# Performance work log

Measured on AMD Instinct MI355X. Metric: run time of the kernel, lower is better.

## Reference

```python
import jax, jax.numpy as jnp
import numpy as np

N_SEQ, MAX_LEN, H_DIM, N_CHAR = 8, 4096, 1024, 256


def setup_inputs() -> dict:
    key = jax.random.key(0)
    ks = jax.random.split(key, 10)
    n_char_ev = 32768
    L, E = 12, 16384
    char_i_seq = jax.random.randint(ks[0], (n_char_ev,), 0, N_SEQ)
    char_i_pos = jax.random.randint(ks[1], (n_char_ev,), 0, MAX_LEN)
    char_ids = jax.random.randint(ks[2], (n_char_ev,), 0, N_CHAR)
    grp_i_seq = jax.random.randint(ks[3], (L, E), 0, N_SEQ)
    grp_i_first = jax.random.randint(ks[4], (L, E), 0, MAX_LEN)
    grp_i_second = jax.random.randint(ks[5], (L, E), 0, MAX_LEN)
    grp_i_pos = jax.random.randint(ks[6], (L, E), 0, MAX_LEN)
    # Learned params: embedding table (std = 1/sqrt(h_dim)) and composer Linear(2h -> h)
    emb_char = jax.random.normal(ks[7], (N_CHAR, H_DIM), dtype=jnp.float32) * (1.0 / H_DIM ** 0.5)
    W = jax.random.normal(ks[8], (2 * H_DIM, H_DIM), dtype=jnp.float32) * (1.0 / (2 * H_DIM) ** 0.5)
    b = jnp.zeros((H_DIM,), dtype=jnp.float32)
    return {"char_i_seq": char_i_seq, "char_i_pos": char_i_pos, "char_ids": char_ids,
            "grp_i_seq": grp_i_seq, "grp_i_first": grp_i_first, "grp_i_second": grp_i_second,
            "grp_i_pos": grp_i_pos, "emb_char": emb_char, "W": W, "b": b}


def reference(char_i_seq, char_i_pos, char_ids, grp_i_seq, grp_i_first,
              grp_i_second, grp_i_pos, emb_char, W, b):
    # h_frag: [n_seq, max_len, h_dim]
    h = jnp.zeros((N_SEQ, MAX_LEN, H_DIM), dtype=emb_char.dtype)
    # Leaf characters: embedding lookup + scatter-add
    h = h.at[char_i_seq, char_i_pos].add(emb_char[char_ids])

    def composer(left, right):
        # tanh(Linear(concat(left, right))) : [E, 2h] @ [2h, h] -> [E, h]
        return jnp.tanh(jnp.concatenate([left, right], axis=-1) @ W + b)

    def level_step(h, idx):
        i_seq, i_first, i_second, i_pos = idx
        out = composer(h[i_seq, i_first], h[i_seq, i_second])  # gather -> compose
        return h.at[i_seq, i_pos].add(out), None                # scatter-add

    h, _ = jax.lax.scan(level_step, h, (grp_i_seq, grp_i_first, grp_i_second, grp_i_pos))
    h = h.at[:, 0].set(0.0)  # h_frag[:, 0].fill_(0)
    return h
```

## Files before the change

### kernel.cpp

```cpp
#include <hip/hip_runtime.h>

#define NS 8
#define ML 4096
#define HD 1024
#define K2 2048
#define NEV 32768
#define NLEV 12
#define NE 16384
#define NSLOT (NS * ML)
#define CAP 8
#define BK 64
#define NT (K2 / BK)
#define LDS_BYTES 131072

typedef __attribute__((ext_vector_type(8))) short bf16x8;
typedef __attribute__((ext_vector_type(4))) float f32x4;

typedef __attribute__((address_space(1))) const void cvoid_g;
typedef __attribute__((address_space(3))) void void_l;

static __device__ __forceinline__ void load_lds_16(const void* g, void* l) {
    __builtin_amdgcn_global_load_lds((cvoid_g*)g, (void_l*)l, 16, 0, 0);
}

static __device__ __forceinline__ unsigned short f2bf(float f) {
    unsigned u = __float_as_uint(f);
    unsigned r = (u + 0x7fffu + ((u >> 16) & 1u)) >> 16;
    return (unsigned short)r;
}

static __device__ __forceinline__ float fast_tanh(float x) {
    return 1.0f - 2.0f / (__expf(2.0f * x) + 1.0f);
}

__global__ void wt_kernel(const float* __restrict__ W, unsigned short* __restrict__ WbT) {
    __shared__ unsigned short tile[64][65];
    const int t = threadIdx.x;
    const int k0 = blockIdx.x * 64;
    const int n0 = blockIdx.y * 64;
#pragma unroll
    for (int i = 0; i < 16; i++) {
        int idx = i * 256 + t;
        int r = idx >> 6, c = idx & 63;
        tile[r][c] = f2bf(W[(size_t)(k0 + r) * HD + n0 + c]);
    }
    __syncthreads();
#pragma unroll
    for (int i = 0; i < 16; i++) {
        int idx = i * 256 + t;
        int r = idx >> 6, c = idx & 63;
        WbT[(size_t)(n0 + r) * K2 + k0 + c] = tile[c][r];
    }
}

__global__ void char_ticket(const int* __restrict__ cseq, const int* __restrict__ cpos,
                            int* __restrict__ counts, int* __restrict__ ticket,
                            int* __restrict__ evlist) {
    const int e = blockIdx.x * 256 + threadIdx.x;
    if (e >= NEV) return;
    const int slot = cseq[e] * ML + cpos[e];
    const int t = atomicAdd(&counts[slot], 1);
    ticket[e] = t;
    if (t < CAP) evlist[slot * CAP + t] = e;
}

__global__ void char_slot_sum(const int* __restrict__ counts, const int* __restrict__ evlist,
                              const int* __restrict__ cid, const float* __restrict__ emb,
                              float* __restrict__ h) {
    const int slot = blockIdx.x;
    const int t = threadIdx.x;
    int n = counts[slot];
    if (n > CAP) n = CAP;
    float4 acc = {0.f, 0.f, 0.f, 0.f};
    for (int i = 0; i < n; i++) {
        const int e = evlist[slot * CAP + i];
        const int id = cid[e];
        const float4 v = ((const float4*)(emb + (size_t)id * HD))[t];
        acc.x += v.x; acc.y += v.y; acc.z += v.z; acc.w += v.w;
    }
    ((float4*)(h + (size_t)slot * HD))[t] = acc;
}

__global__ void char_overflow(const int* __restrict__ cseq, const int* __restrict__ cpos,
                              const int* __restrict__ cid, const int* __restrict__ ticket,
                              const float* __restrict__ emb, float* __restrict__ h) {
    const int e0 = blockIdx.x * 128;
    const int t = threadIdx.x;
    for (int i = 0; i < 128; i++) {
        const int e = e0 + i;
        if (ticket[e] < CAP) continue;
        const int slot = cseq[e] * ML + cpos[e];
        const int id = cid[e];
        const float4 v = ((const float4*)(emb + (size_t)id * HD))[t];
        float* dst = h + (size_t)slot * HD + t * 4;
        atomicAdd(dst + 0, v.x);
        atomicAdd(dst + 1, v.y);
        atomicAdd(dst + 2, v.z);
        atomicAdd(dst + 3, v.w);
    }
}

__global__ void grp_count(const int* __restrict__ iseq, const int* __restrict__ ipos,
                          int* __restrict__ gcounts) {
    const int idx = blockIdx.x * 256 + threadIdx.x;
    if (idx >= NLEV * NE) return;
    const int lev = idx >> 14;
    atomicAdd(&gcounts[lev * NSLOT + iseq[idx] * ML + ipos[idx]], 1);
}

__global__ void grp_dup(const int* __restrict__ iseq, const int* __restrict__ ipos,
                        const int* __restrict__ gcounts, unsigned char* __restrict__ dup) {
    const int idx = blockIdx.x * 256 + threadIdx.x;
    if (idx >= NLEV * NE) return;
    const int lev = idx >> 14;
    dup[idx] = (gcounts[lev * NSLOT + iseq[idx] * ML + ipos[idx]] > 1) ? 1 : 0;
}

__global__ void gather_x(const float* __restrict__ h, const int* __restrict__ iseq,
                         const int* __restrict__ ifirst, const int* __restrict__ isecond,
                         unsigned short* __restrict__ X) {
    const int e = blockIdx.x;
    const int t = threadIdx.x;
    const int seq = iseq[e], f = ifirst[e], s = isecond[e];
    const float4 a = ((const float4*)(h + ((size_t)seq * ML + f) * HD))[t];
    const float4 b = ((const float4*)(h + ((size_t)seq * ML + s) * HD))[t];
    ushort4 pa, pb;
    pa.x = f2bf(a.x); pa.y = f2bf(a.y); pa.z = f2bf(a.z); pa.w = f2bf(a.w);
    pb.x = f2bf(b.x); pb.y = f2bf(b.y); pb.z = f2bf(b.z); pb.w = f2bf(b.w);
    *(ushort4*)(X + (size_t)e * K2 + t * 4) = pa;
    *(ushort4*)(X + (size_t)e * K2 + HD + t * 4) = pb;
}

__global__ __launch_bounds__(512, 2) void gemm_scatter(
    const unsigned short* __restrict__ X,
    const unsigned short* __restrict__ WbT,
    const float* __restrict__ bias,
    const int* __restrict__ iseq, const int* __restrict__ ipos,
    const unsigned char* __restrict__ dup,
    float* __restrict__ h) {
    extern __shared__ unsigned short lds[];
    const int t = threadIdx.x;
    const int lane = t & 63;
    const int w = t >> 6;
    const int wm = w >> 2;
    const int wn = (w & 3) * 64;
    const int fr = lane & 15, fq = lane >> 4;

    const int bid = blockIdx.x;
    const int xcd = bid & 7, bix = bid >> 3;
    const int row0 = ((xcd & 1) * 32 + bix) * 256;
    const int col0 = (xcd >> 1) * 256;

    const int tr = t >> 3;
    const int sp = (t & 7) ^ (tr & 7);
    const unsigned short* Asrc = X + (size_t)(row0 + tr) * K2 + sp * 8;
    const unsigned short* Bsrc = WbT + (size_t)(col0 + tr) * K2 + sp * 8;

    f32x4 acc[8][4];
#pragma unroll
    for (int i = 0; i < 8; i++)
#pragma unroll
        for (int j = 0; j < 4; j++) acc[i][j] = (f32x4){0.f, 0.f, 0.f, 0.f};

    {
        unsigned short* dA = lds;
        unsigned short* dB = lds + 16384;
#pragma unroll
        for (int i = 0; i < 4; i++)
            load_lds_16(Asrc + (size_t)(i * 64) * K2, &dA[(i * 512 + t) * 8]);
#pragma unroll
        for (int i = 0; i < 4; i++)
            load_lds_16(Bsrc + (size_t)(i * 64) * K2, &dB[(i * 512 + t) * 8]);
    }

    for (int kt = 0; kt < NT; kt++) {
        const int d = kt & 1;
        if (kt + 1 < NT) {
            unsigned short* dA = lds + (d ^ 1) * 32768;
            unsigned short* dB = dA + 16384;
            const size_t ko = (size_t)(kt + 1) * BK;
#pragma unroll
            for (int i = 0; i < 4; i++)
                load_lds_16(Asrc + (size_t)(i * 64) * K2 + ko, &dA[(i * 512 + t) * 8]);
#pragma unroll
            for (int i = 0; i < 4; i++)
                load_lds_16(Bsrc + (size_t)(i * 64) * K2 + ko, &dB[(i * 512 + t) * 8]);
            asm volatile("s_waitcnt vmcnt(8)" ::: "memory");
        } else {
            asm volatile("s_waitcnt vmcnt(0)" ::: "memory");
        }
        __builtin_amdgcn_s_barrier();
        asm volatile("" ::: "memory");

        const unsigned short* sA = lds + d * 32768;
        const unsigned short* sB = sA + 16384;
#pragma unroll
        for (int ks = 0; ks < 2; ks++) {
            const int qs = ((ks * 4 + fq) ^ (fr & 7)) * 8;
            bf16x8 af[8], bfr[4];
#pragma unroll
            for (int mt = 0; mt < 8; mt++)
                af[mt] = *(const bf16x8*)&sA[(wm * 128 + mt * 16 + fr) * BK + qs];
#pragma unroll
            for (int nt = 0; nt < 4; nt++)
                bfr[nt] = *(const bf16x8*)&sB[(wn + nt * 16 + fr) * BK + qs];
            __builtin_amdgcn_s_setprio(1);
#pragma unroll
            for (int mt = 0; mt < 8; mt++)
#pragma unroll
                for (int nt = 0; nt < 4; nt++)
                    acc[mt][nt] = __builtin_amdgcn_mfma_f32_16x16x32_bf16(
                        af[mt], bfr[nt], acc[mt][nt], 0, 0, 0);
            __builtin_amdgcn_s_setprio(0);
        }
        asm volatile("" ::: "memory");
        __builtin_amdgcn_s_barrier();
    }

    float bv[4];
#pragma unroll
    for (int ni = 0; ni < 4; ni++) bv[ni] = bias[col0 + wn + ni * 16 + fr];
#pragma unroll
    for (int mi = 0; mi < 8; mi++) {
#pragma unroll
        for (int r = 0; r < 4; r++) {
            const int e = row0 + wm * 128 + mi * 16 + fq * 4 + r;
            const int seq = iseq[e], pos = ipos[e];
            float* hrow = h + ((size_t)seq * ML + pos) * HD + col0 + wn;
            if (dup[e]) {
#pragma unroll
                for (int ni = 0; ni < 4; ni++) {
                    float x = fast_tanh(acc[mi][ni][r] + bv[ni]);
                    atomicAdd(&hrow[ni * 16 + fr], x);
                }
            } else {
#pragma unroll
                for (int ni = 0; ni < 4; ni++) {
                    float x = fast_tanh(acc[mi][ni][r] + bv[ni]);
                    hrow[ni * 16 + fr] += x;
                }
            }
        }
    }
}

__global__ void zero_first(float* __restrict__ h) {
    const int t = blockIdx.x * 256 + threadIdx.x;
    const int seq = t >> 10, d = t & 1023;
    h[(size_t)seq * ML * HD + d] = 0.0f;
}

extern "C" void kernel_launch(void* const* d_in, const int* in_sizes, int n_in,
                              void* d_out, int out_size, void* d_ws, size_t ws_size,
                              hipStream_t stream) {
    const int* char_i_seq = (const int*)d_in[0];
    const int* char_i_pos = (const int*)d_in[1];
    const int* char_ids   = (const int*)d_in[2];
    const int* grp_i_seq    = (const int*)d_in[3];
    const int* grp_i_first  = (const int*)d_in[4];
    const int* grp_i_second = (const int*)d_in[5];
    const int* grp_i_pos    = (const int*)d_in[6];
    const float* emb = (const float*)d_in[7];
    const float* W   = (const float*)d_in[8];
    const float* b   = (const float*)d_in[9];
    float* h = (float*)d_out;

    unsigned short* WbT = (unsigned short*)d_ws;
    unsigned short* X   = (unsigned short*)((char*)d_ws + (8u << 20));
    int* counts = (int*)((char*)d_ws + (72u << 20));
    int* ticket = (int*)((char*)d_ws + (72u << 20) + (1u << 18));
    int* evlist = (int*)((char*)d_ws + (72u << 20) + (1u << 19));
    int* gcounts = (int*)((char*)d_ws + (74u << 20));
    unsigned char* gdup = (unsigned char*)((char*)d_ws + (76u << 20));

    static bool attr_done = false;
    if (!attr_done) {
        (void)hipFuncSetAttribute((const void*)gemm_scatter,
                                  hipFuncAttributeMaxDynamicSharedMemorySize, LDS_BYTES);
        attr_done = true;
    }

    hipMemsetAsync(counts, 0, NSLOT * sizeof(int), stream);
    hipMemsetAsync(gcounts, 0, (size_t)NLEV * NSLOT * sizeof(int), stream);
    wt_kernel<<<dim3(32, 16), 256, 0, stream>>>(W, WbT);
    char_ticket<<<NEV / 256, 256, 0, stream>>>(char_i_seq, char_i_pos, counts, ticket, evlist);
    char_slot_sum<<<NSLOT, 256, 0, stream>>>(counts, evlist, char_ids, emb, h);
    char_overflow<<<NEV / 128, 256, 0, stream>>>(char_i_seq, char_i_pos, char_ids, ticket, emb, h);
    grp_count<<<(NLEV * NE) / 256, 256, 0, stream>>>(grp_i_seq, grp_i_pos, gcounts);
    grp_dup<<<(NLEV * NE) / 256, 256, 0, stream>>>(grp_i_seq, grp_i_pos, gcounts, gdup);

    for (int lev = 0; lev < NLEV; lev++) {
        const int* iseq = grp_i_seq + lev * NE;
        const int* ifir = grp_i_first + lev * NE;
        const int* isec = grp_i_second + lev * NE;
        const int* ipos = grp_i_pos + lev * NE;
        gather_x<<<NE, 256, 0, stream>>>(h, iseq, ifir, isec, X);
        gemm_scatter<<<dim3(256), 512, LDS_BYTES, stream>>>(X, WbT, b, iseq, ipos,
                                                            gdup + lev * NE, h);
    }
    zero_first<<<32, 256, 0, stream>>>(h);
}
```

Measured before the change: 1.578 ms.

## Shrink GEMM tile to 256x128 with BK=32 triple-buffered LDS pipeline

Restructures the per-level GEMM from 256x256 tiles with BK=64 double buffering to 256x128 tiles with BK=32 and a three-stage LDS ring. The grid grows to 512 blocks and LDS drops to 72KB, so more blocks can be resident per CU. Prefetches are issued two k-steps ahead, after the fragment reads, which hides load latency and removes one barrier per iteration. The cost is more A-tile reloads, since each A tile is now fetched by twice as many column blocks, a lower MFMA-to-load ratio per k-step, and a changed block-to-XCD mapping that loses the old L2 locality swizzle.

```diff
diff --git a/kernel.cpp b/kernel.cpp
--- a/kernel.cpp
+++ b/kernel.cpp
@@ -9,9 +9,10 @@
 #define NE 16384
 #define NSLOT (NS * ML)
 #define CAP 8
-#define BK 64
+#define BK 32
 #define NT (K2 / BK)
-#define LDS_BYTES 131072
+#define TILE_ELEMS 12288
+#define LDS_BYTES 73728
 
 typedef __attribute__((ext_vector_type(8))) short bf16x8;
 typedef __attribute__((ext_vector_type(4))) float f32x4;
@@ -131,7 +132,7 @@
     *(ushort4*)(X + (size_t)e * K2 + HD + t * 4) = pb;
 }
 
-__global__ __launch_bounds__(512, 2) void gemm_scatter(
+__global__ __launch_bounds__(512, 4) void gemm_scatter(
     const unsigned short* __restrict__ X,
     const unsigned short* __restrict__ WbT,
     const float* __restrict__ bias,
@@ -143,83 +144,79 @@
     const int lane = t & 63;
     const int w = t >> 6;
     const int wm = w >> 2;
-    const int wn = (w & 3) * 64;
+    const int wn = (w & 3) * 32;
     const int fr = lane & 15, fq = lane >> 4;
 
     const int bid = blockIdx.x;
-    const int xcd = bid & 7, bix = bid >> 3;
-    const int row0 = ((xcd & 1) * 32 + bix) * 256;
-    const int col0 = (xcd >> 1) * 256;
-
-    const int tr = t >> 3;
-    const int sp = (t & 7) ^ (tr & 7);
-    const unsigned short* Asrc = X + (size_t)(row0 + tr) * K2 + sp * 8;
-    const unsigned short* Bsrc = WbT + (size_t)(col0 + tr) * K2 + sp * 8;
-
-    f32x4 acc[8][4];
+    const int col0 = (bid & 7) * 128;
+    const int row0 = (bid >> 3) * 256;
+
+    const int src_c = (t & 3) ^ ((t >> 3) & 3);
+    const unsigned short* Asrc = X + (size_t)(row0 + (t >> 2)) * K2 + src_c * 8;
+    const unsigned short* Bsrc = WbT + (size_t)(col0 + (t >> 2)) * K2 + src_c * 8;
+
+    f32x4 acc[8][2];
 #pragma unroll
     for (int i = 0; i < 8; i++)
 #pragma unroll
-        for (int j = 0; j < 4; j++) acc[i][j] = (f32x4){0.f, 0.f, 0.f, 0.f};
-
-    {
-        unsigned short* dA = lds;
-        unsigned short* dB = lds + 16384;
-#pragma unroll
-        for (int i = 0; i < 4; i++)
-            load_lds_16(Asrc + (size_t)(i * 64) * K2, &dA[(i * 512 + t) * 8]);
-#pragma unroll
-        for (int i = 0; i < 4; i++)
-            load_lds_16(Bsrc + (size_t)(i * 64) * K2, &dB[(i * 512 + t) * 8]);
-    }
+        for (int j = 0; j < 2; j++) acc[i][j] = (f32x4){0.f, 0.f, 0.f, 0.f};
+
+    unsigned short* b0 = lds;
+    unsigned short* b1 = lds + TILE_ELEMS;
+    unsigned short* b2 = lds + 2 * TILE_ELEMS;
+
+    load_lds_16(Asrc, &b0[t * 8]);
+    load_lds_16(Asrc + (size_t)128 * K2, &b0[(512 + t) * 8]);
+    load_lds_16(Bsrc, &b0[8192 + t * 8]);
+    load_lds_16(Asrc + BK, &b1[t * 8]);
+    load_lds_16(Asrc + (size_t)128 * K2 + BK, &b1[(512 + t) * 8]);
+    load_lds_16(Bsrc + BK, &b1[8192 + t * 8]);
+    asm volatile("s_waitcnt vmcnt(3)" ::: "memory");
+    __builtin_amdgcn_s_barrier();
+    asm volatile("" ::: "memory");
+
+    const int slot8 = (fq ^ ((fr >> 1) & 3)) * 8;
 
     for (int kt = 0; kt < NT; kt++) {
-        const int d = kt & 1;
-        if (kt + 1 < NT) {
-            unsigned short* dA = lds + (d ^ 1) * 32768;
-            unsigned short* dB = dA + 16384;
-            const size_t ko = (size_t)(kt + 1) * BK;
-#pragma unroll
-            for (int i = 0; i < 4; i++)
-                load_lds_16(Asrc + (size_t)(i * 64) * K2 + ko, &dA[(i * 512 + t) * 8]);
-#pragma unroll
-            for (int i = 0; i < 4; i++)
-                load_lds_16(Bsrc + (size_t)(i * 64) * K2 + ko, &dB[(i * 512 + t) * 8]);
-            asm volatile("s_waitcnt vmcnt(8)" ::: "memory");
-        } else {
-            asm volatile("s_waitcnt vmcnt(0)" ::: "memory");
+        const unsigned short* sA = b0;
+        const unsigned short* sB = b0 + 8192;
+
+        bf16x8 af[8], bf[2];
+#pragma unroll
+        for (int nt = 0; nt < 2; nt++)
+            bf[nt] = *(const bf16x8*)&sB[(wn + nt * 16 + fr) * BK + slot8];
+#pragma unroll
+        for (int mt = 0; mt < 8; mt++)
+            af[mt] = *(const bf16x8*)&sA[(wm * 128 + mt * 16 + fr) * BK + slot8];
+
+        if (kt + 2 < NT) {
+            const size_t ko = (size_t)(kt + 2) * BK;
+            load_lds_16(Asrc + ko, &b2[t * 8]);
+            load_lds_16(Asrc + (size_t)128 * K2 + ko, &b2[(512 + t) * 8]);
+            load_lds_16(Bsrc + ko, &b2[8192 + t * 8]);
         }
-        __builtin_amdgcn_s_barrier();
-        asm volatile("" ::: "memory");
-
-        const unsigned short* sA = lds + d * 32768;
-        const unsigned short* sB = sA + 16384;
-#pragma unroll
-        for (int ks = 0; ks < 2; ks++) {
-            const int qs = ((ks * 4 + fq) ^ (fr & 7)) * 8;
-            bf16x8 af[8], bfr[4];
-#pragma unroll
-            for (int mt = 0; mt < 8; mt++)
-                af[mt] = *(const bf16x8*)&sA[(wm * 128 + mt * 16 + fr) * BK + qs];
-#pragma unroll
-            for (int nt = 0; nt < 4; nt++)
-                bfr[nt] = *(const bf16x8*)&sB[(wn + nt * 16 + fr) * BK + qs];
-            __builtin_amdgcn_s_setprio(1);
-#pragma unroll
-            for (int mt = 0; mt < 8; mt++)
-#pragma unroll
-                for (int nt = 0; nt < 4; nt++)
-                    acc[mt][nt] = __builtin_amdgcn_mfma_f32_16x16x32_bf16(
-                        af[mt], bfr[nt], acc[mt][nt], 0, 0, 0);
-            __builtin_amdgcn_s_setprio(0);
+
+        __builtin_amdgcn_s_setprio(1);
+#pragma unroll
+        for (int mt = 0; mt < 8; mt++)
+#pragma unroll
+            for (int nt = 0; nt < 2; nt++)
+                acc[mt][nt] = __builtin_amdgcn_mfma_f32_16x16x32_bf16(
+                    af[mt], bf[nt], acc[mt][nt], 0, 0, 0);
+        __builtin_amdgcn_s_setprio(0);
+
+        if (kt < NT - 2)      { asm volatile("s_waitcnt vmcnt(3)" ::: "memory"); }
+        else if (kt == NT - 2){ asm volatile("s_waitcnt vmcnt(0)" ::: "memory"); }
+        if (kt < NT - 1) {
+            __builtin_amdgcn_s_barrier();
+            asm volatile("" ::: "memory");
         }
-        asm volatile("" ::: "memory");
-        __builtin_amdgcn_s_barrier();
-    }
-
-    float bv[4];
-#pragma unroll
-    for (int ni = 0; ni < 4; ni++) bv[ni] = bias[col0 + wn + ni * 16 + fr];
+        unsigned short* tmp = b0; b0 = b1; b1 = b2; b2 = tmp;
+    }
+
+    float bv[2];
+#pragma unroll
+    for (int ni = 0; ni < 2; ni++) bv[ni] = bias[col0 + wn + ni * 16 + fr];
 #pragma unroll
     for (int mi = 0; mi < 8; mi++) {
 #pragma unroll
@@ -229,13 +226,13 @@
             float* hrow = h + ((size_t)seq * ML + pos) * HD + col0 + wn;
             if (dup[e]) {
 #pragma unroll
-                for (int ni = 0; ni < 4; ni++) {
+                for (int ni = 0; ni < 2; ni++) {
                     float x = fast_tanh(acc[mi][ni][r] + bv[ni]);
                     atomicAdd(&hrow[ni * 16 + fr], x);
                 }
             } else {
 #pragma unroll
-                for (int ni = 0; ni < 4; ni++) {
+                for (int ni = 0; ni < 2; ni++) {
                     float x = fast_tanh(acc[mi][ni][r] + bv[ni]);
                     hrow[ni * 16 + fr] += x;
                 }
@@ -295,7 +292,7 @@
         const int* isec = grp_i_second + lev * NE;
         const int* ipos = grp_i_pos + lev * NE;
         gather_x<<<NE, 256, 0, stream>>>(h, iseq, ifir, isec, X);
-        gemm_scatter<<<dim3(256), 512, LDS_BYTES, stream>>>(X, WbT, b, iseq, ipos,
+        gemm_scatter<<<dim3(512), 512, LDS_BYTES, stream>>>(X, WbT, b, iseq, ipos,
                                                             gdup + lev * NE, h);
     }
     zero_first<<<32, 256, 0, stream>>>(h);
```

Measured after the change: 1.832 ms. 1.16x slower.
